# Kernel optimization log

Hardware: AMD Instinct MI355X
Metric: run time of the kernel (lower is better)

Reference implementation:

```python
import jax, jax.numpy as jnp
import numpy as np

NUM_CLASSES = 10
SOFT_CENTER_RADIUS = 3.0
TOPK = 13
IOU_WEIGHT = 3.0
EPS = 1e-07
INF = 100000000.0


def setup_inputs() -> dict:
    key = jax.random.key(0)
    ks = jax.random.split(key, 8)
    B, N, G, C = 8, 16384, 64, NUM_CLASSES
    # priors: [N,4] = (cx, cy, stride_x, stride_y)
    centers = jax.random.uniform(ks[0], (N, 2), minval=0.0, maxval=640.0)
    strides = jnp.full((N, 2), 16.0, dtype=jnp.float32)
    priors = jnp.concatenate([centers, strides], axis=-1)
    # 2D gt boxes (x1,y1,x2,y2) inside a 640px image
    xy = jax.random.uniform(ks[1], (B, G, 2), minval=0.0, maxval=520.0)
    wh = jax.random.uniform(ks[2], (B, G, 2), minval=20.0, maxval=120.0)
    gt_bboxes = jnp.concatenate([xy, xy + wh], axis=-1)
    gt_center = xy + 0.5 * wh
    # 3D boxes: only columns [0,2] (x,z) are used by the dist iou branch
    gt_bboxes_3d = jax.random.normal(ks[3], (B, G, 7)) * 2.0
    pred_bboxes = jax.random.normal(ks[4], (B, N, 7)) * 2.0
    pred_scores = jax.random.normal(ks[5], (B, N, C))
    gt_labels = jax.random.randint(ks[6], (B, G, 1), 0, C, dtype=jnp.int32)
    pad_bbox_flag = jnp.ones((B, G, 1), dtype=jnp.float32)
    return dict(pred_bboxes=pred_bboxes, pred_scores=pred_scores, priors=priors,
                gt_labels=gt_labels, gt_bboxes=gt_bboxes, gt_center=gt_center,
                gt_bboxes_3d=gt_bboxes_3d, pad_bbox_flag=pad_bbox_flag)


def reference(pred_bboxes, pred_scores, priors, gt_labels, gt_bboxes, gt_center,
              gt_bboxes_3d, pad_bbox_flag):
    B, N, _ = pred_bboxes.shape
    G = gt_bboxes.shape[1]

    pc = priors[:, :2]                                   # [N,2]
    # find_inside_points: prior center strictly inside 2D gt box -> [B,N,G]
    cx, cy = pc[None, :, None, 0], pc[None, :, None, 1]
    inside = ((cx > gt_bboxes[:, None, :, 0]) & (cy > gt_bboxes[:, None, :, 1]) &
              (cx < gt_bboxes[:, None, :, 2]) & (cy < gt_bboxes[:, None, :, 3]))
    is_in_gts = inside.astype(jnp.float32) * pad_bbox_flag[:, None, :, 0]  # [B,N,G]
    mask = is_in_gts > 0

    # soft center prior
    strides = priors[None, :, None, 2:]                  # [1,N,1,2]
    diff = (pc[None, :, None, :] - gt_center[:, None, :, :]) / strides
    distance = jnp.linalg.norm(diff, axis=-1) * is_in_gts
    soft_center_prior = 10.0 ** (distance - SOFT_CENTER_RADIUS)

    # dist-type pairwise iou on (x,z) plane
    xz = jnp.array([0, 2])
    pxz = pred_bboxes[:, :, xz]                          # [B,N,2]
    gxz = gt_bboxes_3d[:, :, xz]                         # [B,G,2]
    d = jnp.linalg.norm(pxz[:, :, None, :] - gxz[:, None, :, :], axis=-1)
    pairwise_ious = jnp.clip(1.0 - d / 4.0, 0.0, 1.0)    # [B,N,G]

    iou_cost = -jnp.log(pairwise_ious + EPS) * IOU_WEIGHT

    labels = gt_labels[..., 0]                           # [B,G]
    idx = jnp.broadcast_to(labels[:, None, :], (B, N, G))
    pscores = jnp.take_along_axis(pred_scores, idx, axis=2)  # [B,N,G] logits
    scale = pairwise_ious - jax.nn.sigmoid(pscores)
    # stable BCE-with-logits(pscores, target=pairwise_ious)
    bce = jnp.maximum(pscores, 0.0) - pscores * pairwise_ious + jnp.log1p(jnp.exp(-jnp.abs(pscores)))
    cls_cost = bce * scale ** 2

    cost = jnp.where(mask, cls_cost + iou_cost + soft_center_prior, INF)

    # ---- dynamic k matching ----
    k = min(TOPK, N)
    topk_ious = jax.lax.top_k(jnp.swapaxes(pairwise_ious, 1, 2), k)[0]  # [B,G,k]
    dynamic_ks = jnp.clip(topk_ious.sum(-1).astype(jnp.int32), 1, None)  # [B,G]
    sorted_cost = jnp.sort(cost, axis=1)
    cost_k = jnp.take_along_axis(sorted_cost, dynamic_ks[:, None, :], axis=1)
    cost_k_1 = jnp.take_along_axis(sorted_cost, (dynamic_ks - 1)[:, None, :], axis=1)
    thr = 0.5 * (cost_k + cost_k_1) * is_in_gts          # [B,N,G]
    matching = cost <= thr                               # bool [B,N,G]
    masked_cost = jnp.where(matching, cost, INF)
    multi = matching.sum(-1) > 1                         # prior matched to >1 gt
    argmin_gt = jnp.argmin(masked_cost, axis=2)
    onehot = jax.nn.one_hot(argmin_gt, G, dtype=jnp.bool_)
    matching = jnp.where(multi[..., None], onehot, matching)

    # ---- assemble outputs (dense, jit-friendly version of nonzero indices) ----
    max_index = jnp.argmin(cost, axis=2)                 # [B,N]
    assign_metrics = jnp.take_along_axis(pairwise_ious, max_index[..., None], axis=2)[..., 0]
    matched = matching.any(-1)                           # [B,N]
    gt_idx = jnp.argmax(matching, axis=-1)               # [B,N]
    matched_iou = jnp.take_along_axis(pairwise_ious, gt_idx[..., None], axis=2)[..., 0]
    assign_metrics = jnp.where(matched, matched_iou, assign_metrics)

    assigned_labels = jnp.take_along_axis(labels, max_index, axis=1)  # [B,N]
    assigned_labels = jnp.where(assign_metrics < 1e-07, NUM_CLASSES, assigned_labels)
    assigned_labels = jnp.where(matched, jnp.take_along_axis(labels, gt_idx, axis=1), assigned_labels)

    assigned_labels_weights = jnp.ones((B, N), dtype=jnp.float32)
    return assigned_labels, assigned_labels_weights, assign_metrics, matching
```

## Files before the change

### kernel.cpp

```cpp
#include <hip/hip_runtime.h>
#include <hip/hip_bf16.h>
#include <stdint.h>

#define NCLS 10
#define B_ 8
#define N_ 16384
#define G_ 64
#define INF_ 1.0e8f

typedef unsigned long long u64;
typedef unsigned int u32;

__device__ __forceinline__ u32 ordf(float f) {
    u32 b = __float_as_uint(f);
    return (b & 0x80000000u) ? ~b : (b | 0x80000000u);
}
__device__ __forceinline__ float unordf(u32 u) {
    u32 b = (u & 0x80000000u) ? (u ^ 0x80000000u) : ~u;
    return __uint_as_float(b);
}

__device__ __forceinline__ float iou_pair(float px, float pz, float g3x, float g3z) {
#pragma clang fp contract(off)
    float ddx = px - g3x;
    float ddz = pz - g3z;
    float d = sqrtf(ddx * ddx + ddz * ddz);
    float iou = 1.0f - d / 4.0f;
    return fminf(fmaxf(iou, 0.0f), 1.0f);
}

__device__ __forceinline__ float cost_pair(float cx, float cy, float sx, float sy,
                                           float ps, float gcx, float gcy,
                                           float pad, float iou) {
#pragma clang fp contract(off)
    float dx = (cx - gcx) / sx;
    float dy = (cy - gcy) / sy;
    float dist = sqrtf(dx * dx + dy * dy) * pad;
    float soft = exp10f(dist - 3.0f);
    float iou_cost = -logf(iou + 1e-7f) * 3.0f;
    float e = expf(-fabsf(ps));
    float sig = (ps >= 0.0f) ? (1.0f / (1.0f + e)) : (e / (1.0f + e));
    float scale = iou - sig;
    float bce = fmaxf(ps, 0.0f) - ps * iou + log1pf(e);
    float cls = bce * (scale * scale);
    return cls + iou_cost + soft;
}

__device__ __forceinline__ u32 wave_max_u32(u32 k) {
#pragma unroll
    for (int off = 32; off >= 1; off >>= 1) {
        u32 o = __shfl_xor(k, off, 64);
        k = (o > k) ? o : k;
    }
    return k;
}
__device__ __forceinline__ u32 wave_min_u32(u32 k) {
#pragma unroll
    for (int off = 32; off >= 1; off >>= 1) {
        u32 o = __shfl_xor(k, off, 64);
        k = (o < k) ? o : k;
    }
    return k;
}

__global__ __launch_bounds__(256) void k_ab(
    const float* __restrict__ priors,
    const float* __restrict__ gt_bboxes,
    const float* __restrict__ pad_flag,
    const float* __restrict__ pred_bboxes,
    const float* __restrict__ gt_b3d,
    u64* __restrict__ mask64,
    u64* __restrict__ bitmapT,
    float* __restrict__ iou13)
{
    u32 r5 = blockIdx.x % 5u, q5 = blockIdx.x / 5u;
    int tid = threadIdx.x;
    int lane = tid & 63;
    if (r5 == 4u) {
        int b = q5 >> 6;
        int n = ((q5 & 63) << 8) | tid;
        u32 wword = ((q5 & 63) << 2) | (u32)(tid >> 6);
        float4 pr = ((const float4*)priors)[n];
        float cx = pr.x, cy = pr.y;
        u64 m = 0;
        for (int g = 0; g < G_; ++g) {
            int gi = b * G_ + g;
            float4 gbb = ((const float4*)gt_bboxes)[gi];
            float padv = pad_flag[gi];
            bool isin = (cx > gbb.x) && (cy > gbb.y) && (cx < gbb.z) && (cy < gbb.w)
                        && (padv > 0.0f);
            m |= ((u64)isin) << g;
            u64 bal = __ballot(isin);
            if (lane == 0) bitmapT[(((size_t)gi) << 8) | wword] = bal;
        }
        mask64[(size_t)b * N_ + n] = m;
    } else {
        int c = (int)(q5 * 4u + r5);
        int wid = (c << 2) | (tid >> 6);
        int b = wid >> 10;
        int g = (wid >> 4) & 63;
        int chunk = wid & 15;
        int gi = b * G_ + g;
        float g3x = gt_b3d[gi * 7 + 0];
        float g3z = gt_b3d[gi * 7 + 2];
        const float* pb = pred_bboxes + (size_t)b * N_ * 7;

        float s[16];
        int n0 = chunk * 1024 + lane;
#pragma unroll
        for (int it = 0; it < 16; ++it) {
            int n = n0 + it * 64;
            s[it] = iou_pair(pb[n * 7 + 0], pb[n * 7 + 2], g3x, g3z);
        }
#pragma unroll
        for (int p = 1; p < 16; p <<= 1) {
#pragma unroll
            for (int k = p; k >= 1; k >>= 1) {
#pragma unroll
                for (int j = k % p; j <= 15 - k; j += 2 * k) {
#pragma unroll
                    for (int i = 0; i < k; ++i) {
                        if (i + j + k <= 15) {
                            if ((i + j) / (2 * p) == (i + j + k) / (2 * p)) {
                                float hi = fmaxf(s[i + j], s[i + j + k]);
                                float lo = fminf(s[i + j], s[i + j + k]);
                                s[i + j] = hi; s[i + j + k] = lo;
                            }
                        }
                    }
                }
            }
        }
        float keepv = 0.0f;
        for (int r = 0; r < 13; ++r) {
            u32 mykey = ordf(s[0]);
            u32 m = wave_max_u32(mykey);
            if (lane == r) keepv = unordf(m);
            int winner = __ffsll(__ballot(mykey == m)) - 1;
            if (lane == winner) {
#pragma unroll
                for (int j = 0; j < 13; ++j) s[j] = s[j + 1];
            }
        }
        if (lane < 13) iou13[(size_t)gi * 208 + chunk * 13 + lane] = keepv;
    }
}

__global__ __launch_bounds__(64) void k1c(
    const float* __restrict__ iou13,
    const u64*   __restrict__ bitmapT,
    const float* __restrict__ priors,
    const float* __restrict__ pred_bboxes,
    const float* __restrict__ pred_scores,
    const int*   __restrict__ gt_labels,
    const float* __restrict__ gt_center,
    const float* __restrict__ gt_b3d,
    const float* __restrict__ pad_flag,
    float* __restrict__ thr_half)
{
    int gi = blockIdx.x;
    int lane = threadIdx.x;
    int b = gi >> 6;

    const float* base = iou13 + (size_t)gi * 208;
    float v0 = base[lane];
    float v1 = base[64 + lane];
    float v2 = base[128 + lane];
    float v3 = (lane < 16) ? base[192 + lane] : -3.0e38f;
    { float h = fmaxf(v0, v1), l = fminf(v0, v1); v0 = h; v1 = l; }
    { float h = fmaxf(v2, v3), l = fminf(v2, v3); v2 = h; v3 = l; }
    { float h = fmaxf(v0, v2), l = fminf(v0, v2); v0 = h; v2 = l; }
    { float h = fmaxf(v1, v3), l = fminf(v1, v3); v1 = h; v3 = l; }
    { float h = fmaxf(v1, v2), l = fminf(v1, v2); v1 = h; v2 = l; }
    float sum13 = 0.0f;
    for (int r = 0; r < 13; ++r) {
        u32 mykey = ordf(v0);
        u32 m = wave_max_u32(mykey);
        sum13 += unordf(m);
        int winner = __ffsll(__ballot(mykey == m)) - 1;
        if (lane == winner) { v0 = v1; v1 = v2; v2 = v3; v3 = -3.0e38f; }
    }
    int ks = (int)sum13;
    if (ks < 1) ks = 1;

    float gcx = gt_center[gi * 2 + 0], gcy = gt_center[gi * 2 + 1];
    float g3x = gt_b3d[gi * 7 + 0],   g3z = gt_b3d[gi * 7 + 2];
    float padv = pad_flag[gi];
    int lab = gt_labels[gi];
    const float* pb = pred_bboxes + (size_t)b * N_ * 7;
    const float* sc = pred_scores + (size_t)b * N_ * 10;

    float l[14];
#pragma unroll
    for (int j = 0; j < 14; ++j) l[j] = INF_;
#pragma unroll
    for (int j = 0; j < 4; ++j) {
        u32 w = (u32)(lane + 64 * j);
        u64 wv = bitmapT[(((size_t)gi) << 8) | w];
        u32 nb = w << 6;
        while (wv) {
            int bit = __ffsll(wv) - 1;
            wv &= wv - 1;
            int n = (int)(nb | (u32)bit);
            float4 pr = ((const float4*)priors)[n];
            float px = pb[n * 7 + 0];
            float pz = pb[n * 7 + 2];
            float ps = sc[n * 10 + lab];
            float iou = iou_pair(px, pz, g3x, g3z);
            float cst = cost_pair(pr.x, pr.y, pr.z, pr.w, ps, gcx, gcy, padv, iou);
            if (cst < l[13]) {
                float v = cst;
#pragma unroll
                for (int jj = 0; jj < 14; ++jj) {
                    float o = l[jj]; bool lt = v < o;
                    float mn = lt ? v : o; v = lt ? o : v; l[jj] = mn;
                }
            }
        }
    }
    float ck = INF_, ckm1 = INF_;
    for (int r = 0; r < 14; ++r) {
        u32 mykey = ordf(l[0]);
        u32 m = wave_min_u32(mykey);
        float vm = unordf(m);
        if (r == ks - 1) ckm1 = vm;
        if (r == ks)     ck = vm;
        int winner = __ffsll(__ballot(mykey == m)) - 1;
        if (lane == winner) {
#pragma unroll
            for (int j = 0; j < 13; ++j) l[j] = l[j + 1];
            l[13] = INF_;
        }
    }
    if (lane == 0) thr_half[gi] = 0.5f * (ck + ckm1);
}

__global__ __launch_bounds__(256) void k2(
    const float* __restrict__ priors,
    const float* __restrict__ pred_bboxes,
    const float* __restrict__ pred_scores,
    const int*   __restrict__ gt_labels,
    const float* __restrict__ gt_center,
    const float* __restrict__ gt_b3d,
    const float* __restrict__ pad_flag,
    const float* __restrict__ thr_half,
    const u64*   __restrict__ mask64,
    float* __restrict__ out)
{
    __shared__ float s_gcx[G_], s_gcy[G_], s_g3x[G_], s_g3z[G_];
    __shared__ float s_pad[G_], s_thr[G_];
    __shared__ int   s_lab[G_];
    __shared__ u64   s_words[256];

    int b = blockIdx.x >> 6;
    int n0b = (blockIdx.x & 63) << 8;
    int n = n0b | threadIdx.x;
    size_t t = (size_t)b * N_ + n;

    if (threadIdx.x < G_) {
        int gi = b * G_ + threadIdx.x;
        s_gcx[threadIdx.x] = gt_center[gi * 2 + 0];
        s_gcy[threadIdx.x] = gt_center[gi * 2 + 1];
        s_g3x[threadIdx.x] = gt_b3d[gi * 7 + 0];
        s_g3z[threadIdx.x] = gt_b3d[gi * 7 + 2];
        s_pad[threadIdx.x] = pad_flag[gi];
        s_thr[threadIdx.x] = thr_half[gi];
        s_lab[threadIdx.x] = gt_labels[gi];
    }
    __syncthreads();

    const float* pb = pred_bboxes + (size_t)b * N_ * 7;
    const float* sc = pred_scores + (size_t)b * N_ * 10;
    float4 pr = ((const float4*)priors)[n];
    float px = pb[n * 7 + 0];
    float pz = pb[n * 7 + 2];

    float iouC = iou_pair(px, pz, s_g3x[0], s_g3z[0]);
    float costC = INF_;
    int   labC = s_lab[0];

    float iouM = 0.0f, costM = 3.0e38f;
    int   labM = 0, argM = 0;
    u64 mmatch = 0;

    u64 m = mask64[t];
    while (m) {
        int g = __ffsll(m) - 1;
        m &= m - 1;
        float gcx = s_gcx[g], gcy = s_gcy[g];
        float g3x = s_g3x[g], g3z = s_g3z[g];
        float padg = s_pad[g];
        int   labg = s_lab[g];
        float th = s_thr[g];
        float ps = sc[n * 10 + labg];
        float iou = iou_pair(px, pz, g3x, g3z);
        float c = cost_pair(pr.x, pr.y, pr.z, pr.w, ps, gcx, gcy, padg, iou);
        if (c < costC) { costC = c; iouC = iou; labC = labg; }
        if (c <= th * padg) {
            mmatch |= 1ull << g;
            if (c < costM) { costM = c; iouM = iou; labM = labg; argM = g; }
        }
    }
    int cm = __popcll(mmatch);
    bool matched = cm > 0;
    u64 outm = (cm > 1) ? (1ull << argM) : mmatch;
    float metric = matched ? iouM : iouC;
    float olab = matched ? (float)labM
                         : ((iouC < 1e-7f) ? (float)NCLS : (float)labC);

    float* out_lab = out;
    float* out_w   = out + (size_t)B_ * N_;
    float* out_met = out + (size_t)2 * B_ * N_;
    float* out_mat = out + (size_t)3 * B_ * N_;
    out_lab[t] = olab;
    out_w[t]   = 1.0f;
    out_met[t] = metric;
    s_words[threadIdx.x] = outm;
    __syncthreads();

    int q  = threadIdx.x & 3;
    int r0 = threadIdx.x >> 2;
    size_t rowbase = (size_t)b * N_ + n0b;
#pragma unroll
    for (int it = 0; it < 4; ++it) {
        int row = r0 + (it << 6);
        u64 wv = s_words[row];
        u32 bits = (u32)(wv >> (q * 16)) & 0xffffu;
        float* dst = out_mat + (rowbase + row) * 64 + q * 16;
#pragma unroll
        for (int jj = 0; jj < 4; ++jj) {
            float4 f;
            f.x = (bits >> (jj * 4 + 0)) & 1u ? 1.0f : 0.0f;
            f.y = (bits >> (jj * 4 + 1)) & 1u ? 1.0f : 0.0f;
            f.z = (bits >> (jj * 4 + 2)) & 1u ? 1.0f : 0.0f;
            f.w = (bits >> (jj * 4 + 3)) & 1u ? 1.0f : 0.0f;
            ((float4*)dst)[jj] = f;
        }
    }
}

extern "C" void kernel_launch(void* const* d_in, const int* in_sizes, int n_in,
                              void* d_out, int out_size, void* d_ws, size_t ws_size,
                              hipStream_t stream)
{
    const float* pred_bboxes = (const float*)d_in[0];
    const float* pred_scores = (const float*)d_in[1];
    const float* priors      = (const float*)d_in[2];
    const int*   gt_labels   = (const int*)d_in[3];
    const float* gt_bboxes   = (const float*)d_in[4];
    const float* gt_center   = (const float*)d_in[5];
    const float* gt_b3d      = (const float*)d_in[6];
    const float* pad_flag    = (const float*)d_in[7];
    float* out = (float*)d_out;

    char* ws = (char*)d_ws;
    u64* mask64   = (u64*)ws;
    u64* bitmapT  = (u64*)(ws + 1048576);
    float* iou13  = (float*)(ws + 2097152);
    float* thr_half = (float*)(ws + 2097152 + 425984);

    k_ab<<<2560, 256, 0, stream>>>(priors, gt_bboxes, pad_flag, pred_bboxes,
                                   gt_b3d, mask64, bitmapT, iou13);
    k1c<<<512, 64, 0, stream>>>(iou13, bitmapT, priors, pred_bboxes,
                                pred_scores, gt_labels, gt_center, gt_b3d,
                                pad_flag, thr_half);
    k2<<<512, 256, 0, stream>>>(priors, pred_bboxes, pred_scores, gt_labels,
                                gt_center, gt_b3d, pad_flag,
                                thr_half, mask64, out);
}
```

Before: 81.68 us.

## Compact pred box x,z into float2 buffer and split IoU top-k kernel

Adds a preprocessing pass that gathers the x and z columns of pred_bboxes into a contiguous float2 workspace array. The IoU top-13 stage moves into its own kernel that reads this compact array instead of doing strided 7-float loads, and k1c and k2 read it too. The goal is fewer wasted bytes per load for the repeated reads of pred_bboxes (64 gts per batch each scan all priors). The price is one extra kernel launch and a serial dependency between the compaction and the IoU stage, which previously ran concurrently with the mask computation.

```diff
diff --git a/kernel.cpp b/kernel.cpp
--- a/kernel.cpp
+++ b/kernel.cpp
@@ -63,23 +63,22 @@
     return k;
 }
 
-__global__ __launch_bounds__(256) void k_ab(
+__global__ __launch_bounds__(256) void kP(
     const float* __restrict__ priors,
     const float* __restrict__ gt_bboxes,
     const float* __restrict__ pad_flag,
     const float* __restrict__ pred_bboxes,
-    const float* __restrict__ gt_b3d,
     u64* __restrict__ mask64,
     u64* __restrict__ bitmapT,
-    float* __restrict__ iou13)
-{
-    u32 r5 = blockIdx.x % 5u, q5 = blockIdx.x / 5u;
+    float2* __restrict__ pxz)
+{
     int tid = threadIdx.x;
     int lane = tid & 63;
-    if (r5 == 4u) {
-        int b = q5 >> 6;
-        int n = ((q5 & 63) << 8) | tid;
-        u32 wword = ((q5 & 63) << 2) | (u32)(tid >> 6);
+    if (blockIdx.x < 512) {
+        int q = blockIdx.x;
+        int b = q >> 6;
+        int n = ((q & 63) << 8) | tid;
+        u32 wword = ((q & 63) << 2) | (u32)(tid >> 6);
         float4 pr = ((const float4*)priors)[n];
         float cx = pr.x, cy = pr.y;
         u64 m = 0;
@@ -95,62 +94,78 @@
         }
         mask64[(size_t)b * N_ + n] = m;
     } else {
-        int c = (int)(q5 * 4u + r5);
-        int wid = (c << 2) | (tid >> 6);
-        int b = wid >> 10;
-        int g = (wid >> 4) & 63;
-        int chunk = wid & 15;
-        int gi = b * G_ + g;
-        float g3x = gt_b3d[gi * 7 + 0];
-        float g3z = gt_b3d[gi * 7 + 2];
-        const float* pb = pred_bboxes + (size_t)b * N_ * 7;
-
-        float s[16];
-        int n0 = chunk * 1024 + lane;
-#pragma unroll
-        for (int it = 0; it < 16; ++it) {
-            int n = n0 + it * 64;
-            s[it] = iou_pair(pb[n * 7 + 0], pb[n * 7 + 2], g3x, g3z);
-        }
-#pragma unroll
-        for (int p = 1; p < 16; p <<= 1) {
-#pragma unroll
-            for (int k = p; k >= 1; k >>= 1) {
-#pragma unroll
-                for (int j = k % p; j <= 15 - k; j += 2 * k) {
-#pragma unroll
-                    for (int i = 0; i < k; ++i) {
-                        if (i + j + k <= 15) {
-                            if ((i + j) / (2 * p) == (i + j + k) / (2 * p)) {
-                                float hi = fmaxf(s[i + j], s[i + j + k]);
-                                float lo = fminf(s[i + j], s[i + j + k]);
-                                s[i + j] = hi; s[i + j + k] = lo;
-                            }
+        int base = (int)(blockIdx.x - 512) * 2048 + tid;
+#pragma unroll
+        for (int i = 0; i < 8; ++i) {
+            int idx = base + i * 256;
+            float2 v;
+            v.x = pred_bboxes[(size_t)idx * 7 + 0];
+            v.y = pred_bboxes[(size_t)idx * 7 + 2];
+            pxz[idx] = v;
+        }
+    }
+}
+
+__global__ __launch_bounds__(256) void k1b(
+    const float2* __restrict__ pxz,
+    const float* __restrict__ gt_b3d,
+    float* __restrict__ iou13)
+{
+    int wid = ((int)blockIdx.x << 2) | (threadIdx.x >> 6);
+    int lane = threadIdx.x & 63;
+    int b = wid >> 10;
+    int g = (wid >> 4) & 63;
+    int chunk = wid & 15;
+    int gi = b * G_ + g;
+    float g3x = gt_b3d[gi * 7 + 0];
+    float g3z = gt_b3d[gi * 7 + 2];
+    const float2* pp = pxz + (size_t)b * N_;
+
+    float s[16];
+    int n0 = chunk * 1024 + lane;
+#pragma unroll
+    for (int it = 0; it < 16; ++it) {
+        float2 v = pp[n0 + it * 64];
+        s[it] = iou_pair(v.x, v.y, g3x, g3z);
+    }
+#pragma unroll
+    for (int p = 1; p < 16; p <<= 1) {
+#pragma unroll
+        for (int k = p; k >= 1; k >>= 1) {
+#pragma unroll
+            for (int j = k % p; j <= 15 - k; j += 2 * k) {
+#pragma unroll
+                for (int i = 0; i < k; ++i) {
+                    if (i + j + k <= 15) {
+                        if ((i + j) / (2 * p) == (i + j + k) / (2 * p)) {
+                            float hi = fmaxf(s[i + j], s[i + j + k]);
+                            float lo = fminf(s[i + j], s[i + j + k]);
+                            s[i + j] = hi; s[i + j + k] = lo;
                         }
                     }
                 }
             }
         }
-        float keepv = 0.0f;
-        for (int r = 0; r < 13; ++r) {
-            u32 mykey = ordf(s[0]);
-            u32 m = wave_max_u32(mykey);
-            if (lane == r) keepv = unordf(m);
-            int winner = __ffsll(__ballot(mykey == m)) - 1;
-            if (lane == winner) {
-#pragma unroll
-                for (int j = 0; j < 13; ++j) s[j] = s[j + 1];
-            }
-        }
-        if (lane < 13) iou13[(size_t)gi * 208 + chunk * 13 + lane] = keepv;
-    }
+    }
+    float keepv = 0.0f;
+    for (int r = 0; r < 13; ++r) {
+        u32 mykey = ordf(s[0]);
+        u32 m = wave_max_u32(mykey);
+        if (lane == r) keepv = unordf(m);
+        int winner = __ffsll(__ballot(mykey == m)) - 1;
+        if (lane == winner) {
+#pragma unroll
+            for (int j = 0; j < 13; ++j) s[j] = s[j + 1];
+        }
+    }
+    if (lane < 13) iou13[(size_t)gi * 208 + chunk * 13 + lane] = keepv;
 }
 
 __global__ __launch_bounds__(64) void k1c(
     const float* __restrict__ iou13,
     const u64*   __restrict__ bitmapT,
     const float* __restrict__ priors,
-    const float* __restrict__ pred_bboxes,
+    const float2* __restrict__ pxz,
     const float* __restrict__ pred_scores,
     const int*   __restrict__ gt_labels,
     const float* __restrict__ gt_center,
@@ -187,7 +202,7 @@
     float g3x = gt_b3d[gi * 7 + 0],   g3z = gt_b3d[gi * 7 + 2];
     float padv = pad_flag[gi];
     int lab = gt_labels[gi];
-    const float* pb = pred_bboxes + (size_t)b * N_ * 7;
+    const float2* pp = pxz + (size_t)b * N_;
     const float* sc = pred_scores + (size_t)b * N_ * 10;
 
     float l[14];
@@ -203,17 +218,16 @@
             wv &= wv - 1;
             int n = (int)(nb | (u32)bit);
             float4 pr = ((const float4*)priors)[n];
-            float px = pb[n * 7 + 0];
-            float pz = pb[n * 7 + 2];
+            float2 v = pp[n];
             float ps = sc[n * 10 + lab];
-            float iou = iou_pair(px, pz, g3x, g3z);
+            float iou = iou_pair(v.x, v.y, g3x, g3z);
             float cst = cost_pair(pr.x, pr.y, pr.z, pr.w, ps, gcx, gcy, padv, iou);
             if (cst < l[13]) {
-                float v = cst;
+                float vv = cst;
 #pragma unroll
                 for (int jj = 0; jj < 14; ++jj) {
-                    float o = l[jj]; bool lt = v < o;
-                    float mn = lt ? v : o; v = lt ? o : v; l[jj] = mn;
+                    float o = l[jj]; bool lt = vv < o;
+                    float mn = lt ? vv : o; vv = lt ? o : vv; l[jj] = mn;
                 }
             }
         }
@@ -237,7 +251,7 @@
 
 __global__ __launch_bounds__(256) void k2(
     const float* __restrict__ priors,
-    const float* __restrict__ pred_bboxes,
+    const float2* __restrict__ pxz,
     const float* __restrict__ pred_scores,
     const int*   __restrict__ gt_labels,
     const float* __restrict__ gt_center,
@@ -269,11 +283,11 @@
     }
     __syncthreads();
 
-    const float* pb = pred_bboxes + (size_t)b * N_ * 7;
     const float* sc = pred_scores + (size_t)b * N_ * 10;
     float4 pr = ((const float4*)priors)[n];
-    float px = pb[n * 7 + 0];
-    float pz = pb[n * 7 + 2];
+    float2 v2p = pxz[(size_t)b * N_ + n];
+    float px = v2p.x;
+    float pz = v2p.y;
 
     float iouC = iou_pair(px, pz, s_g3x[0], s_g3z[0]);
     float costC = INF_;
@@ -356,15 +370,17 @@
     char* ws = (char*)d_ws;
     u64* mask64   = (u64*)ws;
     u64* bitmapT  = (u64*)(ws + 1048576);
-    float* iou13  = (float*)(ws + 2097152);
-    float* thr_half = (float*)(ws + 2097152 + 425984);
-
-    k_ab<<<2560, 256, 0, stream>>>(priors, gt_bboxes, pad_flag, pred_bboxes,
-                                   gt_b3d, mask64, bitmapT, iou13);
-    k1c<<<512, 64, 0, stream>>>(iou13, bitmapT, priors, pred_bboxes,
+    float2* pxz   = (float2*)(ws + 2097152);
+    float* iou13  = (float*)(ws + 3145728);
+    float* thr_half = (float*)(ws + 3145728 + 425984);
+
+    kP<<<576, 256, 0, stream>>>(priors, gt_bboxes, pad_flag, pred_bboxes,
+                                mask64, bitmapT, pxz);
+    k1b<<<2048, 256, 0, stream>>>(pxz, gt_b3d, iou13);
+    k1c<<<512, 64, 0, stream>>>(iou13, bitmapT, priors, pxz,
                                 pred_scores, gt_labels, gt_center, gt_b3d,
                                 pad_flag, thr_half);
-    k2<<<512, 256, 0, stream>>>(priors, pred_bboxes, pred_scores, gt_labels,
+    k2<<<512, 256, 0, stream>>>(priors, pxz, pred_scores, gt_labels,
                                 gt_center, gt_b3d, pad_flag,
                                 thr_half, mask64, out);
 }
```

After: 85.72 us. 5.0% more time.
